# Performance work log

Hardware: AMD Instinct MI355X
Metric: run time of the kernel (lower is better)

Reference implementation:

```python
import jax, jax.numpy as jnp
import numpy as np

N = 50000          # nodes
E = 800000         # random edges (self-loops added in reference, per PyG default)
B = 64             # graphs in batch
IN_DIM = 773
HID = 256
OUT = 128
H1, D1 = 4, 64     # heads, head_dim layer 1 (256 = 4*64)
H2, D2 = 4, 32     # heads, head_dim layer 2 (128 = 4*32)
NEG_SLOPE = 0.2


def setup_inputs() -> dict:
    key = jax.random.key(0)
    ks = jax.random.split(key, 20)
    s = 0.02
    x = jax.random.normal(ks[0], (N, IN_DIM), dtype=jnp.float32)
    edge_index = jax.random.randint(ks[1], (2, E), 0, N, dtype=jnp.int32)
    batch = jnp.sort(jax.random.randint(ks[2], (N,), 0, B, dtype=jnp.int32))
    return {
        "x": x,
        "edge_index": edge_index,
        "batch": batch,
        "W_in": jax.random.normal(ks[3], (IN_DIM, HID), jnp.float32) * s,
        "b_in": jnp.zeros((HID,), jnp.float32),
        "W1": jax.random.normal(ks[4], (HID, H1 * D1), jnp.float32) * s,
        "att_src1": jax.random.normal(ks[5], (H1, D1), jnp.float32) * s,
        "att_dst1": jax.random.normal(ks[6], (H1, D1), jnp.float32) * s,
        "b1": jnp.zeros((H1 * D1,), jnp.float32),
        "W2": jax.random.normal(ks[7], (HID, H2 * D2), jnp.float32) * s,
        "att_src2": jax.random.normal(ks[8], (H2, D2), jnp.float32) * s,
        "att_dst2": jax.random.normal(ks[9], (H2, D2), jnp.float32) * s,
        "b2": jnp.zeros((H2 * D2,), jnp.float32),
        "W_cls": jax.random.normal(ks[10], (OUT, 2), jnp.float32) * s,
        "b_cls": jnp.zeros((2,), jnp.float32),
        "W_conf": jax.random.normal(ks[11], (OUT, 1), jnp.float32) * s,
        "b_conf": jnp.zeros((1,), jnp.float32),
    }


def _gat_layer(h, src, dst, W, att_src, att_dst, bias, heads, dim):
    # h: (N, F_in). PyG GATConv, concat=True, eval mode (dropout off).
    hW = (h @ W).reshape(N, heads, dim)                    # (N, H, D)
    a_src = jnp.einsum("nhd,hd->nh", hW, att_src)          # (N, H)
    a_dst = jnp.einsum("nhd,hd->nh", hW, att_dst)
    e = a_src[src] + a_dst[dst]                            # (E', H)
    e = jax.nn.leaky_relu(e, NEG_SLOPE)
    # segment softmax over incoming edges of each dst node
    m = jax.ops.segment_max(e, dst, num_segments=N)        # (N, H)
    ex = jnp.exp(e - m[dst])
    z = jax.ops.segment_sum(ex, dst, num_segments=N)       # (N, H)
    alpha = ex / (z[dst] + 1e-16)                          # (E', H)
    msg = hW[src] * alpha[:, :, None]                      # (E', H, D)
    out = jax.ops.segment_sum(msg, dst, num_segments=N)    # (N, H, D)
    return out.reshape(N, heads * dim) + bias


def reference(x, edge_index, batch, W_in, b_in,
              W1, att_src1, att_dst1, b1,
              W2, att_src2, att_dst2, b2,
              W_cls, b_cls, W_conf, b_conf):
    loops = jnp.arange(N, dtype=edge_index.dtype)
    src = jnp.concatenate([edge_index[0], loops])
    dst = jnp.concatenate([edge_index[1], loops])

    h = jax.nn.relu(x @ W_in + b_in)                       # (N, 256)
    h = jax.nn.relu(_gat_layer(h, src, dst, W1, att_src1, att_dst1, b1, H1, D1))
    h = _gat_layer(h, src, dst, W2, att_src2, att_dst2, b2, H2, D2)
    h = jax.nn.relu(h)                                     # (N, 128)

    # global mean pool over graphs
    sums = jax.ops.segment_sum(h, batch, num_segments=B)   # (B, 128)
    cnts = jax.ops.segment_sum(jnp.ones((N,), h.dtype), batch, num_segments=B)
    graph_emb = sums / jnp.maximum(cnts, 1.0)[:, None]

    class_logits = graph_emb @ W_cls + b_cls               # (B, 2)
    confidence = jax.nn.sigmoid(graph_emb @ W_conf + b_conf)  # (B, 1)
    return class_logits, confidence
```

## Files before the change

kernel.cpp:

```cpp
#include <hip/hip_runtime.h>
#include <math.h>

#define NN 50000
#define NE 800000
#define NB 64
#define IND 773
#define MPAD 50048
#define SCAN_B 196

typedef __attribute__((ext_vector_type(8))) short short8_t;
typedef __attribute__((ext_vector_type(4))) float f32x4;

__device__ __forceinline__ float lrelu(float x) { return x > 0.f ? x : 0.2f * x; }
__device__ __forceinline__ short f2b(float f) {
    unsigned u = __float_as_uint(f);
    unsigned r = (u + 0x7fffu + ((u >> 16) & 1u)) >> 16;
    return (short)r;
}
__device__ __forceinline__ float b2f(short s) {
    return __uint_as_float(((unsigned)(unsigned short)s) << 16);
}

#define GLOAD16(g, l) __builtin_amdgcn_global_load_lds(                         \
    (const __attribute__((address_space(1))) void*)(g),                         \
    (__attribute__((address_space(3))) void*)(l), 16, 0, 0)

__global__ __launch_bounds__(512) void gemm_a(const float* __restrict__ X,
                                              const short* __restrict__ Bt,
                                              const float* __restrict__ bias,
                                              short* __restrict__ C) {
    const int K = 800, N = 256, NT = 25;
    __shared__ short As[2][128 * 32];
    __shared__ short Bs[2][256 * 32];
    const int t = threadIdx.x;
    const int w = t >> 6, l = t & 63;
    const int l15 = l & 15, lh = l >> 4;
    const int bm = blockIdx.x * 128;
    const int wr = (w >> 2) * 64, wc = (w & 3) * 64;
    const int arow = t >> 2, acb = (t & 3) * 8;
    const int gm = bm + arow;
    const bool rowok = gm < NN;
    const float* xrow = X + (size_t)gm * IND;
    const short* bG = Bt + (size_t)(t >> 2) * K + (t & 3) * 8;

    f32x4 acc[4][4];
#pragma unroll
    for (int i = 0; i < 4; ++i)
#pragma unroll
        for (int j = 0; j < 4; ++j) acc[i][j] = (f32x4){0.f, 0.f, 0.f, 0.f};

    short8_t rA;
    auto loadA = [&](int it) {
        int gk = it * 32 + acb;
        if (rowok && gk + 7 < IND) {
            float4 v0 = *(const float4*)(xrow + gk);
            float4 v1 = *(const float4*)(xrow + gk + 4);
            rA[0] = f2b(v0.x); rA[1] = f2b(v0.y); rA[2] = f2b(v0.z); rA[3] = f2b(v0.w);
            rA[4] = f2b(v1.x); rA[5] = f2b(v1.y); rA[6] = f2b(v1.z); rA[7] = f2b(v1.w);
        } else {
#pragma unroll
            for (int j = 0; j < 8; ++j)
                rA[j] = (rowok && gk + j < IND) ? f2b(xrow[gk + j]) : (short)0;
        }
    };
    auto stageB = [&](int buf, int it) {
        GLOAD16(bG + it * 32, &Bs[buf][w * 512]);
        GLOAD16(bG + (size_t)128 * K + it * 32, &Bs[buf][128 * 32 + w * 512]);
    };

    loadA(0);
    stageB(0, 0);
    stageB(1, 1);
    *(short8_t*)&As[0][arow * 32 + acb] = rA;
    loadA(1);
    __syncthreads();

    for (int it = 0; it < NT; ++it) {
        const int c = it & 1, n = c ^ 1;
        short8_t af[4], bfr[4];
#pragma unroll
        for (int mi = 0; mi < 4; ++mi)
            af[mi] = *(const short8_t*)&As[c][(wr + mi * 16 + l15) * 32 + lh * 8];
#pragma unroll
        for (int ni = 0; ni < 4; ++ni)
            bfr[ni] = *(const short8_t*)&Bs[c][(wc + ni * 16 + l15) * 32 + lh * 8];
        if (it + 1 < NT) *(short8_t*)&As[n][arow * 32 + acb] = rA;
#pragma unroll
        for (int mi = 0; mi < 4; ++mi)
#pragma unroll
            for (int ni = 0; ni < 4; ++ni)
                acc[mi][ni] = __builtin_amdgcn_mfma_f32_16x16x32_bf16(af[mi], bfr[ni], acc[mi][ni], 0, 0, 0);
        __syncthreads();
        if (it + 2 < NT) {
            loadA(it + 2);
            stageB(c, it + 2);
        }
    }

#pragma unroll
    for (int mi = 0; mi < 4; ++mi) {
#pragma unroll
        for (int r = 0; r < 4; ++r) {
            int grow = bm + wr + mi * 16 + lh * 4 + r;
            if (grow >= NN) continue;
#pragma unroll
            for (int ni = 0; ni < 4; ++ni) {
                int gcol = wc + ni * 16 + l15;
                float v = fmaxf(acc[mi][ni][r] + bias[gcol], 0.f);
                C[(size_t)grow * N + gcol] = f2b(v);
            }
        }
    }
}

__global__ __launch_bounds__(256) void gemm_b(const short* __restrict__ A,
                                              const short* __restrict__ Bt,
                                              const float* __restrict__ att_s,
                                              const float* __restrict__ att_d,
                                              short* __restrict__ C,
                                              float* __restrict__ a_s,
                                              float* __restrict__ a_d) {
    const int K = 256, N = 256, NT = 8;
    __shared__ short As[2][128 * 32];
    __shared__ short Bs[2][128 * 32];
    const int t = threadIdx.x;
    const int w = t >> 6, l = t & 63;
    const int l15 = l & 15, lh = l >> 4;
    const int bm = blockIdx.x * 128, bn = blockIdx.y * 128;
    const int wr = (w >> 1) * 64, wc = (w & 1) * 64;

    const short* aG = A + (size_t)(bm + w * 32 + (l >> 2)) * K + (l & 3) * 8;
    const short* bG = Bt + (size_t)(bn + w * 32 + (l >> 2)) * K + (l & 3) * 8;

    auto stage = [&](int buf, int k0) {
        GLOAD16(aG + k0, As[buf] + (w * 32) * 32);
        GLOAD16(aG + (size_t)16 * K + k0, As[buf] + (w * 32 + 16) * 32);
        GLOAD16(bG + k0, Bs[buf] + (w * 32) * 32);
        GLOAD16(bG + (size_t)16 * K + k0, Bs[buf] + (w * 32 + 16) * 32);
    };

    f32x4 acc[4][4];
#pragma unroll
    for (int i = 0; i < 4; ++i)
#pragma unroll
        for (int j = 0; j < 4; ++j) acc[i][j] = (f32x4){0.f, 0.f, 0.f, 0.f};

    stage(0, 0);
    stage(1, 32);
    __syncthreads();

    for (int it = 0; it < NT; ++it) {
        const int c = it & 1;
        short8_t af[4], bfr[4];
#pragma unroll
        for (int mi = 0; mi < 4; ++mi)
            af[mi] = *(const short8_t*)&As[c][(wr + mi * 16 + l15) * 32 + lh * 8];
#pragma unroll
        for (int ni = 0; ni < 4; ++ni)
            bfr[ni] = *(const short8_t*)&Bs[c][(wc + ni * 16 + l15) * 32 + lh * 8];
#pragma unroll
        for (int mi = 0; mi < 4; ++mi)
#pragma unroll
            for (int ni = 0; ni < 4; ++ni)
                acc[mi][ni] = __builtin_amdgcn_mfma_f32_16x16x32_bf16(af[mi], bfr[ni], acc[mi][ni], 0, 0, 0);
        __syncthreads();
        if (it + 2 < NT) stage(c, (it + 2) * 32);
    }

    const int head = (bn + wc) >> 6;
    float sa[4], sd[4];
#pragma unroll
    for (int ni = 0; ni < 4; ++ni) {
        sa[ni] = att_s[head * 64 + ni * 16 + l15];
        sd[ni] = att_d[head * 64 + ni * 16 + l15];
    }
#pragma unroll
    for (int mi = 0; mi < 4; ++mi) {
#pragma unroll
        for (int r = 0; r < 4; ++r) {
            int grow = bm + wr + mi * 16 + lh * 4 + r;
            float s = acc[mi][0][r] * sa[0] + acc[mi][1][r] * sa[1] +
                      acc[mi][2][r] * sa[2] + acc[mi][3][r] * sa[3];
            float d = acc[mi][0][r] * sd[0] + acc[mi][1][r] * sd[1] +
                      acc[mi][2][r] * sd[2] + acc[mi][3][r] * sd[3];
#pragma unroll
            for (int off = 1; off < 16; off <<= 1) {
                s += __shfl_xor(s, off);
                d += __shfl_xor(d, off);
            }
            if (grow < NN) {
                if (l15 == 0) { a_s[grow * 4 + head] = s; a_d[grow * 4 + head] = d; }
#pragma unroll
                for (int ni = 0; ni < 4; ++ni)
                    C[(size_t)grow * N + bn + wc + ni * 16 + l15] = f2b(acc[mi][ni][r]);
            }
        }
    }
}

__global__ __launch_bounds__(256) void gemm_c(const short* __restrict__ A,
                                              const short* __restrict__ Bt,
                                              const float* __restrict__ att_s,
                                              const float* __restrict__ att_d,
                                              short* __restrict__ C,
                                              float* __restrict__ a_s,
                                              float* __restrict__ a_d) {
    const int K = 256, N = 128, NT = 8;
    __shared__ short As[2][128 * 32];
    __shared__ short Bs[2][128 * 32];
    const int t = threadIdx.x;
    const int w = t >> 6, l = t & 63;
    const int l15 = l & 15, lh = l >> 4;
    const int bm = blockIdx.x * 128;
    const int wr = (w >> 1) * 64, wc = (w & 1) * 64;

    const short* aG = A + (size_t)(bm + w * 32 + (l >> 2)) * K + (l & 3) * 8;
    const short* bG = Bt + (size_t)(w * 32 + (l >> 2)) * K + (l & 3) * 8;

    auto stage = [&](int buf, int k0) {
        GLOAD16(aG + k0, As[buf] + (w * 32) * 32);
        GLOAD16(aG + (size_t)16 * K + k0, As[buf] + (w * 32 + 16) * 32);
        GLOAD16(bG + k0, Bs[buf] + (w * 32) * 32);
        GLOAD16(bG + (size_t)16 * K + k0, Bs[buf] + (w * 32 + 16) * 32);
    };

    f32x4 acc[4][4];
#pragma unroll
    for (int i = 0; i < 4; ++i)
#pragma unroll
        for (int j = 0; j < 4; ++j) acc[i][j] = (f32x4){0.f, 0.f, 0.f, 0.f};

    stage(0, 0);
    stage(1, 32);
    __syncthreads();

    for (int it = 0; it < NT; ++it) {
        const int c = it & 1;
        short8_t af[4], bfr[4];
#pragma unroll
        for (int mi = 0; mi < 4; ++mi)
            af[mi] = *(const short8_t*)&As[c][(wr + mi * 16 + l15) * 32 + lh * 8];
#pragma unroll
        for (int ni = 0; ni < 4; ++ni)
            bfr[ni] = *(const short8_t*)&Bs[c][(wc + ni * 16 + l15) * 32 + lh * 8];
#pragma unroll
        for (int mi = 0; mi < 4; ++mi)
#pragma unroll
            for (int ni = 0; ni < 4; ++ni)
                acc[mi][ni] = __builtin_amdgcn_mfma_f32_16x16x32_bf16(af[mi], bfr[ni], acc[mi][ni], 0, 0, 0);
        __syncthreads();
        if (it + 2 < NT) stage(c, (it + 2) * 32);
    }

    const int h0 = wc >> 5;
    float sa[4], sd[4];
#pragma unroll
    for (int ni = 0; ni < 4; ++ni) {
        int idx = (h0 + (ni >> 1)) * 32 + (ni & 1) * 16 + l15;
        sa[ni] = att_s[idx];
        sd[ni] = att_d[idx];
    }
#pragma unroll
    for (int mi = 0; mi < 4; ++mi) {
#pragma unroll
        for (int r = 0; r < 4; ++r) {
            int grow = bm + wr + mi * 16 + lh * 4 + r;
            float s0 = acc[mi][0][r] * sa[0] + acc[mi][1][r] * sa[1];
            float s1 = acc[mi][2][r] * sa[2] + acc[mi][3][r] * sa[3];
            float d0 = acc[mi][0][r] * sd[0] + acc[mi][1][r] * sd[1];
            float d1 = acc[mi][2][r] * sd[2] + acc[mi][3][r] * sd[3];
#pragma unroll
            for (int off = 1; off < 16; off <<= 1) {
                s0 += __shfl_xor(s0, off); s1 += __shfl_xor(s1, off);
                d0 += __shfl_xor(d0, off); d1 += __shfl_xor(d1, off);
            }
            if (grow < NN) {
                if (l15 == 0) {
                    a_s[grow * 4 + h0] = s0; a_s[grow * 4 + h0 + 1] = s1;
                    a_d[grow * 4 + h0] = d0; a_d[grow * 4 + h0 + 1] = d1;
                }
#pragma unroll
                for (int ni = 0; ni < 4; ++ni)
                    C[(size_t)grow * N + wc + ni * 16 + l15] = f2b(acc[mi][ni][r]);
            }
        }
    }
}

__global__ __launch_bounds__(256) void k_wt_t(const float* __restrict__ W,
                                              short* __restrict__ Wt,
                                              int K, int N, int Kp) {
    __shared__ short tile[32][33];
    int kb = blockIdx.x * 32, nb = blockIdx.y * 32;
    int tx = threadIdx.x & 31, ty = threadIdx.x >> 5;
#pragma unroll
    for (int r = 0; r < 32; r += 8) {
        int k = kb + ty + r;
        tile[ty + r][tx] = (k < K) ? f2b(W[(size_t)k * N + nb + tx]) : (short)0;
    }
    __syncthreads();
#pragma unroll
    for (int r = 0; r < 32; r += 8) {
        int n = nb + ty + r, k = kb + tx;
        Wt[(size_t)n * Kp + k] = tile[tx][ty + r];
    }
}

__global__ __launch_bounds__(256) void k_zero(int* __restrict__ p, int n) {
    int i = blockIdx.x * 256 + threadIdx.x;
    if (i < n) p[i] = 0;
}

__global__ void k_hist(const int* __restrict__ ei, int* __restrict__ deg) {
    int e = blockIdx.x * 256 + threadIdx.x;
    if (e >= NE) return;
    atomicAdd(&deg[ei[NE + e]], 1);
}

__global__ __launch_bounds__(256) void k_bsum(const int* __restrict__ deg,
                                              int* __restrict__ bsum) {
    int i = blockIdx.x * 256 + threadIdx.x;
    int v = (i < NN) ? deg[i] : 0;
#pragma unroll
    for (int off = 32; off; off >>= 1) v += __shfl_down(v, off);
    __shared__ int ws[4];
    if ((threadIdx.x & 63) == 0) ws[threadIdx.x >> 6] = v;
    __syncthreads();
    if (threadIdx.x == 0) bsum[blockIdx.x] = ws[0] + ws[1] + ws[2] + ws[3];
}

__global__ __launch_bounds__(256) void k_bscan(const int* __restrict__ bsum,
                                               int* __restrict__ boff) {
    int t = threadIdx.x;
    int orig = (t < SCAN_B) ? bsum[t] : 0;
    int v = orig;
    int lane = t & 63, wid = t >> 6;
#pragma unroll
    for (int off = 1; off < 64; off <<= 1) {
        int u = __shfl_up(v, off);
        if (lane >= off) v += u;
    }
    __shared__ int ws[4];
    if (lane == 63) ws[wid] = v;
    __syncthreads();
    int add = 0;
    for (int wq = 0; wq < wid; ++wq) add += ws[wq];
    if (t < SCAN_B) boff[t] = v + add - orig;
}

__global__ __launch_bounds__(256) void k_scan3(const int* __restrict__ deg,
                                               const int* __restrict__ boff,
                                               int* __restrict__ rowp,
                                               int* __restrict__ cursor) {
    int b = blockIdx.x;
    int i = b * 256 + threadIdx.x;
    int d = (i < NN) ? deg[i] : 0;
    int v = d;
    int lane = threadIdx.x & 63, wid = threadIdx.x >> 6;
#pragma unroll
    for (int off = 1; off < 64; off <<= 1) {
        int u = __shfl_up(v, off);
        if (lane >= off) v += u;
    }
    __shared__ int ws[4];
    if (lane == 63) ws[wid] = v;
    __syncthreads();
    int add = boff[b];
    for (int wq = 0; wq < wid; ++wq) add += ws[wq];
    int excl = add + v - d;
    if (i < NN) { rowp[i] = excl; cursor[i] = excl; }
    if (i == NN - 1) rowp[NN] = excl + d;
}

__global__ void k_scatter(const int* __restrict__ ei, int* __restrict__ cursor,
                          int* __restrict__ colidx) {
    int e = blockIdx.x * 256 + threadIdx.x;
    if (e >= NE) return;
    int s = ei[e], d = ei[NE + e];
    int pos = atomicAdd(&cursor[d], 1);
    colidx[pos] = s;
}

template<int HD>
__global__ __launch_bounds__(256) void gat_agg(const short* __restrict__ hW,
                                               const float* __restrict__ a_s,
                                               const float* __restrict__ a_d,
                                               const int* __restrict__ row_ptr,
                                               const int* __restrict__ colidx,
                                               const float* __restrict__ bias,
                                               short* __restrict__ outp) {
    const int CPL = HD / 64;
    int node = blockIdx.x * 4 + (threadIdx.x >> 6);
    int lane = threadIdx.x & 63;
    if (node >= NN) return;
    int h = lane >> 4;
    int start = row_ptr[node], end = row_ptr[node + 1];
    float adst = a_d[node * 4 + h];
    float eself = lrelu(a_s[node * 4 + h] + adst);

    float z = 1.f;
    float acc[CPL];
    {
        const short* row = hW + (size_t)node * HD + lane * CPL;
        if (CPL == 4) { short4 q = *(const short4*)row; acc[0]=b2f(q.x); acc[1]=b2f(q.y); acc[2]=b2f(q.z); acc[3]=b2f(q.w); }
        else          { short2 q = *(const short2*)row; acc[0]=b2f(q.x); acc[1]=b2f(q.y); }
    }
    for (int e = start; e < end; e += 8) {
        int sidx[8];
        float xs[8], ex[8];
#pragma unroll
        for (int q = 0; q < 8; ++q) {
            int ee = e + q;
            sidx[q] = colidx[ee < end ? ee : end - 1];
        }
#pragma unroll
        for (int q = 0; q < 8; ++q) xs[q] = a_s[sidx[q] * 4 + h];
        float v[8][CPL];
        if (CPL == 4) {
#pragma unroll
            for (int q = 0; q < 8; ++q) {
                short4 qq = *(const short4*)(hW + (size_t)sidx[q] * HD + lane * 4);
                v[q][0]=b2f(qq.x); v[q][1]=b2f(qq.y); v[q][2]=b2f(qq.z); v[q][3]=b2f(qq.w);
            }
        } else {
#pragma unroll
            for (int q = 0; q < 8; ++q) {
                short2 qq = *(const short2*)(hW + (size_t)sidx[q] * HD + lane * 2);
                v[q][0]=b2f(qq.x); v[q][1]=b2f(qq.y);
            }
        }
#pragma unroll
        for (int q = 0; q < 8; ++q) {
            float w = __expf(lrelu(xs[q] + adst) - eself);
            ex[q] = (e + q < end) ? w : 0.f;
        }
#pragma unroll
        for (int q = 0; q < 8; ++q) z += ex[q];
#pragma unroll
        for (int j = 0; j < CPL; ++j) {
            float a = 0.f;
#pragma unroll
            for (int q = 0; q < 8; ++q) a += ex[q] * v[q][j];
            acc[j] += a;
        }
    }
    float inv = 1.f / z;
    short* orow = outp + (size_t)node * HD + lane * CPL;
#pragma unroll
    for (int j = 0; j < CPL; ++j)
        orow[j] = f2b(fmaxf(acc[j] * inv + bias[lane * CPL + j], 0.f));
}

__global__ __launch_bounds__(512) void pool_head(const short* __restrict__ h2,
                                                 const int* __restrict__ batch,
                                                 const float* __restrict__ W_cls,
                                                 const float* __restrict__ b_cls,
                                                 const float* __restrict__ W_conf,
                                                 const float* __restrict__ b_conf,
                                                 float* __restrict__ out) {
    int b = blockIdx.x;
    int t = threadIdx.x & 127;
    int g = threadIdx.x >> 7;
    int lo = 0, hi = NN;
    while (lo < hi) { int mid = (lo + hi) >> 1; if (batch[mid] < b) lo = mid + 1; else hi = mid; }
    int start = lo;
    lo = 0; hi = NN;
    while (lo < hi) { int mid = (lo + hi) >> 1; if (batch[mid] < b + 1) lo = mid + 1; else hi = mid; }
    int end = lo;

    float acc = 0.f;
    for (int n = start + g; n < end; n += 4) acc += b2f(h2[(size_t)n * 128 + t]);
    __shared__ float se[4][128];
    se[g][t] = acc;
    __syncthreads();
    if (g == 0) {
        float emb = (se[0][t] + se[1][t] + se[2][t] + se[3][t]) /
                    fmaxf((float)(end - start), 1.f);
        se[0][t] = emb;
    }
    __syncthreads();
    if (threadIdx.x == 0) {
        float v = b_cls[0];
        for (int c = 0; c < 128; ++c) v += se[0][c] * W_cls[c * 2 + 0];
        out[b * 2 + 0] = v;
    } else if (threadIdx.x == 1) {
        float v = b_cls[1];
        for (int c = 0; c < 128; ++c) v += se[0][c] * W_cls[c * 2 + 1];
        out[b * 2 + 1] = v;
    } else if (threadIdx.x == 2) {
        float v = b_conf[0];
        for (int c = 0; c < 128; ++c) v += se[0][c] * W_conf[c];
        out[128 + b] = 1.f / (1.f + expf(-v));
    }
}

extern "C" void kernel_launch(void* const* d_in, const int* in_sizes, int n_in,
                              void* d_out, int out_size, void* d_ws, size_t ws_size,
                              hipStream_t stream) {
    const float* x        = (const float*)d_in[0];
    const int*   ei       = (const int*)d_in[1];
    const int*   batch    = (const int*)d_in[2];
    const float* W_in     = (const float*)d_in[3];
    const float* b_in     = (const float*)d_in[4];
    const float* W1       = (const float*)d_in[5];
    const float* att_src1 = (const float*)d_in[6];
    const float* att_dst1 = (const float*)d_in[7];
    const float* b1       = (const float*)d_in[8];
    const float* W2       = (const float*)d_in[9];
    const float* att_src2 = (const float*)d_in[10];
    const float* att_dst2 = (const float*)d_in[11];
    const float* b2       = (const float*)d_in[12];
    const float* W_cls    = (const float*)d_in[13];
    const float* b_cls    = (const float*)d_in[14];
    const float* W_conf   = (const float*)d_in[15];
    const float* b_conf   = (const float*)d_in[16];
    float* out = (float*)d_out;

    char* ws = (char*)d_ws;
    short* h0  = (short*)(ws + 0);
    short* hW1 = (short*)(ws + 25624576);
    short* h1  = (short*)(ws + 51249152);
    short* hW2 = (short*)(ws + 76873728);
    short* h2  = (short*)(ws + 89686016);
    size_t base = 102498304;
    short* Wt_in = (short*)(ws + base);
    short* Wt1   = (short*)(ws + base + 409600);
    short* Wt2   = (short*)(ws + base + 540672);
    float* a_s1  = (float*)(ws + base + 606208);
    float* a_d1  = (float*)(ws + base + 1406208);
    int*   deg    = (int*)(ws + base + 2206208);
    int*   rowp   = (int*)(ws + base + 2406208);
    int*   cursor = (int*)(ws + base + 2606272);
    int*   colidx = (int*)(ws + base + 2806272);
    int*   bsum   = (int*)(ws + base + 6006272);
    int*   boff   = (int*)(ws + base + 6007296);

    k_wt_t<<<dim3(25, 8), 256, 0, stream>>>(W_in, Wt_in, IND, 256, 800);
    k_wt_t<<<dim3(8, 8), 256, 0, stream>>>(W1, Wt1, 256, 256, 256);
    k_wt_t<<<dim3(8, 4), 256, 0, stream>>>(W2, Wt2, 256, 128, 256);

    k_zero<<<SCAN_B, 256, 0, stream>>>(deg, NN);
    k_hist<<<NE / 256, 256, 0, stream>>>(ei, deg);
    k_bsum<<<SCAN_B, 256, 0, stream>>>(deg, bsum);
    k_bscan<<<1, 256, 0, stream>>>(bsum, boff);
    k_scan3<<<SCAN_B, 256, 0, stream>>>(deg, boff, rowp, cursor);
    k_scatter<<<NE / 256, 256, 0, stream>>>(ei, cursor, colidx);

    gemm_a<<<391, 512, 0, stream>>>(x, Wt_in, b_in, h0);
    gemm_b<<<dim3(391, 2), 256, 0, stream>>>(h0, Wt1, att_src1, att_dst1, hW1, a_s1, a_d1);
    gat_agg<256><<<12500, 256, 0, stream>>>(hW1, a_s1, a_d1, rowp, colidx, b1, h1);
    gemm_c<<<391, 256, 0, stream>>>(h1, Wt2, att_src2, att_dst2, hW2, a_s1, a_d1);
    gat_agg<128><<<12500, 256, 0, stream>>>(hW2, a_s1, a_d1, rowp, colidx, b2, h2);
    pool_head<<<NB, 512, 0, stream>>>(h2, batch, W_cls, b_cls, W_conf, b_conf, out);
}
```

Baseline: 379.0 us.

## Store GAT projected features in FP8 and merge small prep kernels

The projected node features hW1/hW2 are now stored as FP8 (e4m3 via cvt_pk_fp8) instead of bf16. They are staged through LDS so global writes are coalesced 16-byte stores, and the aggregation kernels decode FP8 when gathering. This halves the bytes moved in the random-access gather over neighbors, at a cost in precision. Separately, the three weight-transpose launches and the degree zeroing are merged into one kernel, and the single-block scan is folded into k_scan3, which cuts launch count.

```diff
diff --git a/kernel.cpp b/kernel.cpp
--- a/kernel.cpp
+++ b/kernel.cpp
@@ -10,6 +10,7 @@
 
 typedef __attribute__((ext_vector_type(8))) short short8_t;
 typedef __attribute__((ext_vector_type(4))) float f32x4;
+typedef __attribute__((ext_vector_type(2))) float f32x2;
 
 __device__ __forceinline__ float lrelu(float x) { return x > 0.f ? x : 0.2f * x; }
 __device__ __forceinline__ short f2b(float f) {
@@ -19,6 +20,18 @@
 }
 __device__ __forceinline__ float b2f(short s) {
     return __uint_as_float(((unsigned)(unsigned short)s) << 16);
+}
+__device__ __forceinline__ unsigned char enc8(float v) {
+    return (unsigned char)(__builtin_amdgcn_cvt_pk_fp8_f32(v, v, 0, false) & 0xff);
+}
+__device__ __forceinline__ void dec4(unsigned w, float* v) {
+    f32x2 lo = __builtin_amdgcn_cvt_pk_f32_fp8((int)w, false);
+    f32x2 hi = __builtin_amdgcn_cvt_pk_f32_fp8((int)w, true);
+    v[0] = lo[0]; v[1] = lo[1]; v[2] = hi[0]; v[3] = hi[1];
+}
+__device__ __forceinline__ void dec2(unsigned w, float* v) {
+    f32x2 lo = __builtin_amdgcn_cvt_pk_f32_fp8((int)w, false);
+    v[0] = lo[0]; v[1] = lo[1];
 }
 
 #define GLOAD16(g, l) __builtin_amdgcn_global_load_lds(                         \
@@ -117,7 +130,7 @@
                                               const short* __restrict__ Bt,
                                               const float* __restrict__ att_s,
                                               const float* __restrict__ att_d,
-                                              short* __restrict__ C,
+                                              unsigned char* __restrict__ C8,
                                               float* __restrict__ a_s,
                                               float* __restrict__ a_d) {
     const int K = 256, N = 256, NT = 8;
@@ -174,11 +187,13 @@
         sa[ni] = att_s[head * 64 + ni * 16 + l15];
         sd[ni] = att_d[head * 64 + ni * 16 + l15];
     }
+    char* R = (char*)As;
 #pragma unroll
     for (int mi = 0; mi < 4; ++mi) {
 #pragma unroll
         for (int r = 0; r < 4; ++r) {
-            int grow = bm + wr + mi * 16 + lh * 4 + r;
+            int rloc = wr + mi * 16 + lh * 4 + r;
+            int grow = bm + rloc;
             float s = acc[mi][0][r] * sa[0] + acc[mi][1][r] * sa[1] +
                       acc[mi][2][r] * sa[2] + acc[mi][3][r] * sa[3];
             float d = acc[mi][0][r] * sd[0] + acc[mi][1][r] * sd[1] +
@@ -188,13 +203,20 @@
                 s += __shfl_xor(s, off);
                 d += __shfl_xor(d, off);
             }
-            if (grow < NN) {
-                if (l15 == 0) { a_s[grow * 4 + head] = s; a_d[grow * 4 + head] = d; }
-#pragma unroll
-                for (int ni = 0; ni < 4; ++ni)
-                    C[(size_t)grow * N + bn + wc + ni * 16 + l15] = f2b(acc[mi][ni][r]);
-            }
-        }
+            if (grow < NN && l15 == 0) { a_s[grow * 4 + head] = s; a_d[grow * 4 + head] = d; }
+#pragma unroll
+            for (int ni = 0; ni < 4; ++ni)
+                R[rloc * 128 + wc + ni * 16 + l15] = (char)enc8(acc[mi][ni][r]);
+        }
+    }
+    __syncthreads();
+#pragma unroll
+    for (int i = 0; i < 4; ++i) {
+        int idx = i * 256 + t;
+        int row = idx >> 3, cb = (idx & 7) * 16;
+        int grow = bm + row;
+        if (grow < NN)
+            *(float4*)&C8[(size_t)grow * N + bn + cb] = *(float4*)&R[row * 128 + cb];
     }
 }
 
@@ -202,7 +224,7 @@
                                               const short* __restrict__ Bt,
                                               const float* __restrict__ att_s,
                                               const float* __restrict__ att_d,
-                                              short* __restrict__ C,
+                                              unsigned char* __restrict__ C8,
                                               float* __restrict__ a_s,
                                               float* __restrict__ a_d) {
     const int K = 256, N = 128, NT = 8;
@@ -260,11 +282,13 @@
         sa[ni] = att_s[idx];
         sd[ni] = att_d[idx];
     }
+    char* R = (char*)As;
 #pragma unroll
     for (int mi = 0; mi < 4; ++mi) {
 #pragma unroll
         for (int r = 0; r < 4; ++r) {
-            int grow = bm + wr + mi * 16 + lh * 4 + r;
+            int rloc = wr + mi * 16 + lh * 4 + r;
+            int grow = bm + rloc;
             float s0 = acc[mi][0][r] * sa[0] + acc[mi][1][r] * sa[1];
             float s1 = acc[mi][2][r] * sa[2] + acc[mi][3][r] * sa[3];
             float d0 = acc[mi][0][r] * sd[0] + acc[mi][1][r] * sd[1];
@@ -274,24 +298,44 @@
                 s0 += __shfl_xor(s0, off); s1 += __shfl_xor(s1, off);
                 d0 += __shfl_xor(d0, off); d1 += __shfl_xor(d1, off);
             }
-            if (grow < NN) {
-                if (l15 == 0) {
-                    a_s[grow * 4 + h0] = s0; a_s[grow * 4 + h0 + 1] = s1;
-                    a_d[grow * 4 + h0] = d0; a_d[grow * 4 + h0 + 1] = d1;
-                }
-#pragma unroll
-                for (int ni = 0; ni < 4; ++ni)
-                    C[(size_t)grow * N + wc + ni * 16 + l15] = f2b(acc[mi][ni][r]);
+            if (grow < NN && l15 == 0) {
+                a_s[grow * 4 + h0] = s0; a_s[grow * 4 + h0 + 1] = s1;
+                a_d[grow * 4 + h0] = d0; a_d[grow * 4 + h0 + 1] = d1;
             }
-        }
-    }
-}
-
-__global__ __launch_bounds__(256) void k_wt_t(const float* __restrict__ W,
-                                              short* __restrict__ Wt,
-                                              int K, int N, int Kp) {
+#pragma unroll
+            for (int ni = 0; ni < 4; ++ni)
+                R[rloc * 128 + wc + ni * 16 + l15] = (char)enc8(acc[mi][ni][r]);
+        }
+    }
+    __syncthreads();
+#pragma unroll
+    for (int i = 0; i < 4; ++i) {
+        int idx = i * 256 + t;
+        int row = idx >> 3, cb = (idx & 7) * 16;
+        int grow = bm + row;
+        if (grow < NN)
+            *(float4*)&C8[(size_t)grow * N + cb] = *(float4*)&R[row * 128 + cb];
+    }
+}
+
+__global__ __launch_bounds__(256) void k_prep(const float* __restrict__ W_in,
+                                              const float* __restrict__ W1,
+                                              const float* __restrict__ W2,
+                                              short* __restrict__ Wt_in,
+                                              short* __restrict__ Wt1,
+                                              short* __restrict__ Wt2,
+                                              int* __restrict__ deg) {
+    int b = blockIdx.x;
+    const float* W; short* Wt; int K, N, Kp, kb, nb;
+    if (b < 200)      { W = W_in; Wt = Wt_in; K = IND; N = 256; Kp = 800; kb = (b % 25) * 32; nb = (b / 25) * 32; }
+    else if (b < 264) { b -= 200; W = W1; Wt = Wt1; K = 256; N = 256; Kp = 256; kb = (b % 8) * 32; nb = (b / 8) * 32; }
+    else if (b < 296) { b -= 264; W = W2; Wt = Wt2; K = 256; N = 128; Kp = 256; kb = (b % 8) * 32; nb = (b / 8) * 32; }
+    else {
+        int i = (b - 296) * 256 + threadIdx.x;
+        if (i < NN) deg[i] = 0;
+        return;
+    }
     __shared__ short tile[32][33];
-    int kb = blockIdx.x * 32, nb = blockIdx.y * 32;
     int tx = threadIdx.x & 31, ty = threadIdx.x >> 5;
 #pragma unroll
     for (int r = 0; r < 32; r += 8) {
@@ -304,11 +348,6 @@
         int n = nb + ty + r, k = kb + tx;
         Wt[(size_t)n * Kp + k] = tile[tx][ty + r];
     }
-}
-
-__global__ __launch_bounds__(256) void k_zero(int* __restrict__ p, int n) {
-    int i = blockIdx.x * 256 + threadIdx.x;
-    if (i < n) p[i] = 0;
 }
 
 __global__ void k_hist(const int* __restrict__ ei, int* __restrict__ deg) {
@@ -329,32 +368,15 @@
     if (threadIdx.x == 0) bsum[blockIdx.x] = ws[0] + ws[1] + ws[2] + ws[3];
 }
 
-__global__ __launch_bounds__(256) void k_bscan(const int* __restrict__ bsum,
-                                               int* __restrict__ boff) {
-    int t = threadIdx.x;
-    int orig = (t < SCAN_B) ? bsum[t] : 0;
-    int v = orig;
-    int lane = t & 63, wid = t >> 6;
-#pragma unroll
-    for (int off = 1; off < 64; off <<= 1) {
-        int u = __shfl_up(v, off);
-        if (lane >= off) v += u;
-    }
-    __shared__ int ws[4];
-    if (lane == 63) ws[wid] = v;
-    __syncthreads();
-    int add = 0;
-    for (int wq = 0; wq < wid; ++wq) add += ws[wq];
-    if (t < SCAN_B) boff[t] = v + add - orig;
-}
-
 __global__ __launch_bounds__(256) void k_scan3(const int* __restrict__ deg,
-                                               const int* __restrict__ boff,
+                                               const int* __restrict__ bsum,
                                                int* __restrict__ rowp,
                                                int* __restrict__ cursor) {
     int b = blockIdx.x;
     int i = b * 256 + threadIdx.x;
     int d = (i < NN) ? deg[i] : 0;
+    __shared__ int sb[SCAN_B];
+    if (threadIdx.x < SCAN_B) sb[threadIdx.x] = bsum[threadIdx.x];
     int v = d;
     int lane = threadIdx.x & 63, wid = threadIdx.x >> 6;
 #pragma unroll
@@ -365,7 +387,8 @@
     __shared__ int ws[4];
     if (lane == 63) ws[wid] = v;
     __syncthreads();
-    int add = boff[b];
+    int add = 0;
+    for (int q = 0; q < b; ++q) add += sb[q];
     for (int wq = 0; wq < wid; ++wq) add += ws[wq];
     int excl = add + v - d;
     if (i < NN) { rowp[i] = excl; cursor[i] = excl; }
@@ -382,7 +405,7 @@
 }
 
 template<int HD>
-__global__ __launch_bounds__(256) void gat_agg(const short* __restrict__ hW,
+__global__ __launch_bounds__(256) void gat_agg(const unsigned char* __restrict__ hW8,
                                                const float* __restrict__ a_s,
                                                const float* __restrict__ a_d,
                                                const int* __restrict__ row_ptr,
@@ -401,9 +424,9 @@
     float z = 1.f;
     float acc[CPL];
     {
-        const short* row = hW + (size_t)node * HD + lane * CPL;
-        if (CPL == 4) { short4 q = *(const short4*)row; acc[0]=b2f(q.x); acc[1]=b2f(q.y); acc[2]=b2f(q.z); acc[3]=b2f(q.w); }
-        else          { short2 q = *(const short2*)row; acc[0]=b2f(q.x); acc[1]=b2f(q.y); }
+        const unsigned char* row = hW8 + (size_t)node * HD + lane * CPL;
+        if (CPL == 4) dec4(*(const unsigned*)row, acc);
+        else          dec2(*(const unsigned short*)row, acc);
     }
     for (int e = start; e < end; e += 8) {
         int sidx[8];
@@ -418,21 +441,17 @@
         float v[8][CPL];
         if (CPL == 4) {
 #pragma unroll
-            for (int q = 0; q < 8; ++q) {
-                short4 qq = *(const short4*)(hW + (size_t)sidx[q] * HD + lane * 4);
-                v[q][0]=b2f(qq.x); v[q][1]=b2f(qq.y); v[q][2]=b2f(qq.z); v[q][3]=b2f(qq.w);
-            }
+            for (int q = 0; q < 8; ++q)
+                dec4(*(const unsigned*)(hW8 + (size_t)sidx[q] * HD + lane * 4), v[q]);
         } else {
 #pragma unroll
-            for (int q = 0; q < 8; ++q) {
-                short2 qq = *(const short2*)(hW + (size_t)sidx[q] * HD + lane * 2);
-                v[q][0]=b2f(qq.x); v[q][1]=b2f(qq.y);
-            }
+            for (int q = 0; q < 8; ++q)
+                dec2(*(const unsigned short*)(hW8 + (size_t)sidx[q] * HD + lane * 2), v[q]);
         }
 #pragma unroll
         for (int q = 0; q < 8; ++q) {
-            float w = __expf(lrelu(xs[q] + adst) - eself);
-            ex[q] = (e + q < end) ? w : 0.f;
+            float wq = __expf(lrelu(xs[q] + adst) - eself);
+            ex[q] = (e + q < end) ? wq : 0.f;
         }
 #pragma unroll
         for (int q = 0; q < 8; ++q) z += ex[q];
@@ -517,12 +536,12 @@
     float* out = (float*)d_out;
 
     char* ws = (char*)d_ws;
-    short* h0  = (short*)(ws + 0);
-    short* hW1 = (short*)(ws + 25624576);
-    short* h1  = (short*)(ws + 51249152);
-    short* hW2 = (short*)(ws + 76873728);
-    short* h2  = (short*)(ws + 89686016);
-    size_t base = 102498304;
+    short*         h0   = (short*)(ws + 0);
+    unsigned char* hW1  = (unsigned char*)(ws + 25624576);
+    short*         h1   = (short*)(ws + 38436864);
+    unsigned char* hW2  = (unsigned char*)(ws + 64061440);
+    short*         h2   = (short*)(ws + 70467584);
+    size_t base = 83279872;
     short* Wt_in = (short*)(ws + base);
     short* Wt1   = (short*)(ws + base + 409600);
     short* Wt2   = (short*)(ws + base + 540672);
@@ -533,17 +552,11 @@
     int*   cursor = (int*)(ws + base + 2606272);
     int*   colidx = (int*)(ws + base + 2806272);
     int*   bsum   = (int*)(ws + base + 6006272);
-    int*   boff   = (int*)(ws + base + 6007296);
-
-    k_wt_t<<<dim3(25, 8), 256, 0, stream>>>(W_in, Wt_in, IND, 256, 800);
-    k_wt_t<<<dim3(8, 8), 256, 0, stream>>>(W1, Wt1, 256, 256, 256);
-    k_wt_t<<<dim3(8, 4), 256, 0, stream>>>(W2, Wt2, 256, 128, 256);
-
-    k_zero<<<SCAN_B, 256, 0, stream>>>(deg, NN);
+
+    k_prep<<<296 + SCAN_B, 256, 0, stream>>>(W_in, W1, W2, Wt_in, Wt1, Wt2, deg);
     k_hist<<<NE / 256, 256, 0, stream>>>(ei, deg);
     k_bsum<<<SCAN_B, 256, 0, stream>>>(deg, bsum);
-    k_bscan<<<1, 256, 0, stream>>>(bsum, boff);
-    k_scan3<<<SCAN_B, 256, 0, stream>>>(deg, boff, rowp, cursor);
+    k_scan3<<<SCAN_B, 256, 0, stream>>>(deg, bsum, rowp, cursor);
     k_scatter<<<NE / 256, 256, 0, stream>>>(ei, cursor, colidx);
 
     gemm_a<<<391, 512, 0, stream>>>(x, Wt_in, b_in, h0);
```

Result: faster. 347.0 us (-8.5%).
